# Kernel optimization log

Hardware: AMD Instinct MI355X
Metric: run time of the kernel (lower is better)

## Reference

```python
import jax, jax.numpy as jnp
import numpy as np

BN_EPS = 1e-5
LEAKY_SLOPE = 0.1


def conv_bn_leaky(x, w, gamma, beta, mean, var, pad):
    # Conv2d(no bias) + BatchNorm2d(inference) + LeakyReLU(0.1), NCHW/OIHW
    y = jax.lax.conv_general_dilated(
        x, w, window_strides=(1, 1), padding=[(pad, pad), (pad, pad)],
        dimension_numbers=("NCHW", "OIHW", "NCHW"))
    scale = gamma / jnp.sqrt(var + BN_EPS)
    shift = beta - mean * scale
    y = y * scale[None, :, None, None] + shift[None, :, None, None]
    return jnp.where(y > 0, y, LEAKY_SLOPE * y)


def reorg(x, s=2):
    # vedanet Reorg: out[b, (a*s+d)*C + c, i, j] = x[b, c, i*s+a, j*s+d]
    B, C, H, W = x.shape
    Ho, Wo = H // s, W // s
    return x.reshape(B, C, Ho, s, Wo, s).transpose(0, 3, 5, 1, 2, 4).reshape(B, s * s * C, Ho, Wo)


def setup_inputs() -> dict:
    key = jax.random.key(0)
    ks = jax.random.split(key, 10)
    B, H, W = 32, 19, 19
    NC, NA = 20, 5
    return {
        "stage6": jax.random.normal(ks[0], (B, 1024, H, W), jnp.float32),
        "stage5": jax.random.normal(ks[1], (B, 512, 2 * H, 2 * W), jnp.float32),
        "w1": jax.random.normal(ks[2], (64, 512, 1, 1), jnp.float32) * 0.05,
        "g1": jnp.ones((64,), jnp.float32),
        "b1": jnp.zeros((64,), jnp.float32),
        "m1": jax.random.normal(ks[3], (64,), jnp.float32) * 0.1,
        "v1": jax.random.uniform(ks[4], (64,), jnp.float32, 0.5, 1.5),
        "w2": jax.random.normal(ks[5], (1024, 1280, 3, 3), jnp.float32) * 0.02,
        "g2": jnp.ones((1024,), jnp.float32),
        "b2": jnp.zeros((1024,), jnp.float32),
        "m2": jax.random.normal(ks[6], (1024,), jnp.float32) * 0.1,
        "v2": jax.random.uniform(ks[7], (1024,), jnp.float32, 0.5, 1.5),
        "meta_state": jax.random.normal(ks[8], (NC, NA * 6, 1025), jnp.float32) * 0.05,
    }


def reference(stage6, stage5, w1, g1, b1, m1, v1, w2, g2, b2, m2, v2, meta_state):
    # layers[0]: 1x1 conv-bn-leaky on stage5, then Reorg(2) -> (B, 256, H, W)
    x = conv_bn_leaky(stage5, w1, g1, b1, m1, v1, pad=0)
    x = reorg(x, 2)
    # layers[1]: 3x3 conv-bn-leaky on concat -> (B, 1024, H, W)
    pre = conv_bn_leaky(jnp.concatenate([x, stage6], axis=1), w2, g2, b2, m2, v2, pad=1)
    # meta_predict: per-class 1x1 conv, batched as one einsum
    cls_w = meta_state[:, :, :-1]   # (NC, NA*6, 1024)
    cls_b = meta_state[:, :, -1]    # (NC, NA*6)
    out = jnp.einsum("bkij,cmk->bcmij", pre, cls_w) + cls_b[None, :, :, None, None]
    B, NC, M = pre.shape[0], meta_state.shape[0], meta_state.shape[1]
    return out.reshape(B * NC, M, pre.shape[2], pre.shape[3])
```

## Files before the change

kernel.cpp:

```cpp
#include <hip/hip_runtime.h>

typedef unsigned short u16;
typedef unsigned int   u32;

typedef __attribute__((ext_vector_type(8))) short bf16x8;
typedef __attribute__((ext_vector_type(4))) float f32x4;

__device__ __forceinline__ u16 f2bf(float f) {
  u32 u = __float_as_uint(f);
  u32 r = (u + 0x7fffu + ((u >> 16) & 1u)) >> 16;
  return (u16)r;
}

__device__ __forceinline__ void async16(const void* g, void* l) {
  __builtin_amdgcn_global_load_lds(
      (const __attribute__((address_space(1))) u32*)g,
      (__attribute__((address_space(3))) u32*)l, 16, 0, 0);
}

__global__ __launch_bounds__(256) void mega_prep_kern(
    const float* __restrict__ stage5, const float* __restrict__ s6,
    const float* __restrict__ w1,
    const float* __restrict__ g1, const float* __restrict__ b1,
    const float* __restrict__ m1, const float* __restrict__ v1,
    const float* __restrict__ w2, const float* __restrict__ g2,
    const float* __restrict__ b2, const float* __restrict__ m2,
    const float* __restrict__ v2, const float* __restrict__ meta,
    u16* __restrict__ in_bf, u16* __restrict__ w2p,
    u16* __restrict__ clsp, float* __restrict__ clsb,
    float* __restrict__ shift2)
{
  __shared__ __align__(16) char smem[18816];
  const int bid = blockIdx.x;
  const int t = threadIdx.x;

  if (bid < 722) {
    float* sc_s = (float*)smem;
    float* sh_s = (float*)(smem + 256);
    char*  aT   = smem + 512;
    char*  bT   = smem + 4608;
    const int w = t >> 6, lane = t & 63;
    if (t < 64) {
      float s = g1[t] * rsqrtf(v1[t] + 1e-5f);
      sc_s[t] = s;
      sh_s[t] = b1[t] - m1[t] * s;
    }
    const int m0 = bid * 64;
    const int pS = t & 63, gS = t >> 6;
    const int mS = m0 + pS;
    const int bS = mS / 1444, hwS = mS - bS * 1444;
    const float* s5 = stage5 + (size_t)bS * (512 * 1444) + hwS;
    const int ocA = t >> 2, icqA = t & 3;
    const float* w1r = w1 + (size_t)ocA * 512 + icqA * 8;
    char* aW = aT + (ocA >> 4) * 1024 + (icqA * 16 + (ocA & 15)) * 16;
    char* bW = bT + pS * 64 + ((gS ^ ((pS >> 1) & 3))) * 16;
    const int bR = (w * 16 + (lane & 15)) * 64 +
                   (((lane >> 4) ^ (((lane & 15) >> 1) & 3))) * 16;
    f32x4 acc[4] = {};
    __syncthreads();
    const float sA = sc_s[ocA];
    for (int kc = 0; kc < 16; ++kc) {
      const int ic0 = kc * 32;
      float a8[8], b8[8];
#pragma unroll
      for (int e = 0; e < 8; ++e) a8[e] = w1r[ic0 + e];
#pragma unroll
      for (int e = 0; e < 8; ++e) b8[e] = s5[(size_t)(ic0 + gS * 8 + e) * 1444];
      __syncthreads();
      uint4 av, bv;
      av.x = (u32)f2bf(a8[0] * sA) | ((u32)f2bf(a8[1] * sA) << 16);
      av.y = (u32)f2bf(a8[2] * sA) | ((u32)f2bf(a8[3] * sA) << 16);
      av.z = (u32)f2bf(a8[4] * sA) | ((u32)f2bf(a8[5] * sA) << 16);
      av.w = (u32)f2bf(a8[6] * sA) | ((u32)f2bf(a8[7] * sA) << 16);
      bv.x = (u32)f2bf(b8[0]) | ((u32)f2bf(b8[1]) << 16);
      bv.y = (u32)f2bf(b8[2]) | ((u32)f2bf(b8[3]) << 16);
      bv.z = (u32)f2bf(b8[4]) | ((u32)f2bf(b8[5]) << 16);
      bv.w = (u32)f2bf(b8[6]) | ((u32)f2bf(b8[7]) << 16);
      *(uint4*)aW = av;
      *(uint4*)bW = bv;
      __syncthreads();
      bf16x8 bfv = *(const bf16x8*)(bT + bR);
#pragma unroll
      for (int i = 0; i < 4; ++i) {
        bf16x8 af = *(const bf16x8*)(aT + i * 1024 + lane * 16);
        acc[i] = __builtin_amdgcn_mfma_f32_16x16x32_bf16(af, bfv, acc[i], 0, 0, 0);
      }
    }
    const int mE = m0 + w * 16 + (lane & 15);
    const int bE = mE / 1444, hwE = mE - bE * 1444;
    const int h = hwE / 38, wq = hwE - h * 38;
    const int ho = h >> 1, wo = wq >> 1, q = ((h & 1) << 1) | (wq & 1);
    u16* dst = in_bf + (((size_t)bE * 21 + 1 + ho) * 21 + 1 + wo) * 1280 + q * 64;
    const int lq = lane >> 4;
#pragma unroll
    for (int i = 0; i < 4; ++i) {
      int oc = i * 16 + lq * 4;
      float v0 = acc[i][0] + sh_s[oc + 0]; v0 = v0 > 0.f ? v0 : 0.1f * v0;
      float v1_ = acc[i][1] + sh_s[oc + 1]; v1_ = v1_ > 0.f ? v1_ : 0.1f * v1_;
      float v2_ = acc[i][2] + sh_s[oc + 2]; v2_ = v2_ > 0.f ? v2_ : 0.1f * v2_;
      float v3 = acc[i][3] + sh_s[oc + 3]; v3 = v3 > 0.f ? v3 : 0.1f * v3;
      u32 lo = (u32)f2bf(v0) | ((u32)f2bf(v1_) << 16);
      u32 hi = (u32)f2bf(v2_) | ((u32)f2bf(v3) << 16);
      u32* dp = (u32*)(dst + oc);
      dp[0] = lo; dp[1] = hi;
    }
    return;
  }

  if (bid < 3794) {
    u16 (*tile)[66] = (u16(*)[66])smem;
    const int sub = bid - 722;
    const int jt = sub % 6, ct = (sub / 6) % 16, b = sub / 96;
    const int ij0 = jt * 64, c0 = ct * 64;
    const int col = t & 63, rr = t >> 6;
#pragma unroll
    for (int r = 0; r < 16; ++r) {
      int cl = r * 4 + rr;
      int ij = ij0 + col;
      float v = 0.f;
      if (ij < 361) v = s6[((size_t)b * 1024 + c0 + cl) * 361 + ij];
      tile[cl][col] = f2bf(v);
    }
    __syncthreads();
#pragma unroll
    for (int r = 0; r < 16; ++r) {
      int ijl = r * 4 + rr;
      int ij = ij0 + ijl;
      if (ij < 361) {
        int i = ij / 19, j = ij - i * 19;
        in_bf[(((size_t)b * 21 + 1 + i) * 21 + 1 + j) * 1280 + 256 + c0 + col] =
            tile[col][ijl];
      }
    }
    return;
  }

  if (bid < 5394) {
    int gi = (bid - 3794) * 256 + t;
    int b = gi / 12800;
    int rem = gi - b * 12800;
    int p = rem / 160, qq = rem - p * 160;
    int row, col;
    if (p < 21)      { row = 0;      col = p; }
    else if (p < 42) { row = 20;     col = p - 21; }
    else if (p < 61) { row = p - 41; col = 0; }
    else             { row = p - 60; col = 20; }
    uint4 z = {0u, 0u, 0u, 0u};
    *(uint4*)(in_bf + (((size_t)b * 21 + row) * 21 + col) * 1280 + qq * 8) = z;
    return;
  }

  if (bid < 5694) {
    int idx = (bid - 5394) * 256 + t;
    int cm = idx >> 7, a = idx & 127;
    int kc = a >> 2, ksub = a & 3;
    int tile_ = cm >> 7, g = (cm >> 4) & 7, mm = cm & 15;
    const float* srcp = meta + (size_t)cm * 1025 + a * 8;
    uint4 v;
    v.x = (u32)f2bf(srcp[0]) | ((u32)f2bf(srcp[1]) << 16);
    v.y = (u32)f2bf(srcp[2]) | ((u32)f2bf(srcp[3]) << 16);
    v.z = (u32)f2bf(srcp[4]) | ((u32)f2bf(srcp[5]) << 16);
    v.w = (u32)f2bf(srcp[6]) | ((u32)f2bf(srcp[7]) << 16);
    size_t dst = (((size_t)tile_ * 32 + kc) * 8 + g) * 512
                 + (size_t)(ksub * 16 + mm) * 8;
    *(uint4*)(clsp + dst) = v;
    if (idx < 600) clsb[idx] = meta[(size_t)idx * 1025 + 1024];
    if (idx < 1024) {
      float sc = g2[idx] * rsqrtf(v2[idx] + 1e-5f);
      shift2[idx] = b2[idx] - m2[idx] * sc;
    }
    return;
  }

  {
    u16* tile = (u16*)smem;
    float* sc_s = (float*)(smem + 18720);
    const int sub = bid - 5694;
    const int icb = sub % 10;
    const int oc0 = (sub / 10) * 8;
    if (t < 8) sc_s[t] = g2[oc0 + t] * rsqrtf(v2[oc0 + t] + 1e-5f);
    __syncthreads();
    const float* src = w2 + (size_t)oc0 * 11520 + (size_t)icb * 128 * 9;
#pragma unroll
    for (int r = 0; r < 36; ++r) {
      int p = r * 256 + t;
      int oc_l = p / 1152, rem = p - oc_l * 1152;
      int ic_l = rem / 9, khw = rem - ic_l * 9;
      tile[oc_l * 1170 + khw * 130 + ic_l] =
          f2bf(src[(size_t)oc_l * 11520 + rem] * sc_s[oc_l]);
    }
    __syncthreads();
#pragma unroll
    for (int r = 0; r < 5; ++r) {
      int wi = r * 256 + t;
      if (wi < 1152) {
        int oc_l = wi / 144, q = wi - oc_l * 144;
        int khw = q >> 4, c = (q >> 2) & 3, ksub = q & 3;
        int oc = oc0 + oc_l;
        int kt = khw * 40 + icb * 4 + c;
        const u16* s = &tile[oc_l * 1170 + khw * 130 + c * 32 + ksub * 8];
        uint4 v;
        v.x = (u32)s[0] | ((u32)s[1] << 16);
        v.y = (u32)s[2] | ((u32)s[3] << 16);
        v.z = (u32)s[4] | ((u32)s[5] << 16);
        v.w = (u32)s[6] | ((u32)s[7] << 16);
        size_t dst = (((size_t)(oc >> 8) * 360 + kt) * 2 + ((oc & 255) >> 7)) * 4096
                     + (size_t)(((oc >> 4) & 7) * 64 + ksub * 16 + (oc & 15)) * 8;
        *(uint4*)(w2p + dst) = v;
      }
    }
  }
}

__global__ __launch_bounds__(512, 2) void conv2_gemm_kern(
    const u16* __restrict__ Wp, const u16* __restrict__ Ig,
    const float* __restrict__ shift2, u16* __restrict__ pre)
{
  __shared__ u16 As[4][8192];
  __shared__ u16 Bs[4][8192];
  __shared__ float shft[256];

  const int t = threadIdx.x;
  const int w = t >> 6, lane = t & 63;
  const int wm = w >> 2, wn = w & 3;

  const int s = ((blockIdx.x & 7) * 23) + (blockIdx.x >> 3);
  const int mTile = s >> 2, ocTile = s & 3;
  const int m0 = mTile * 256, oc0 = ocTile * 256;

  const int rw = t >> 2;
  const int rpart = ((t & 3) ^ ((t >> 3) & 3)) * 8;
  int mA = m0 + rw;        if (mA > 11551) mA = 11551;
  int mB = m0 + 128 + rw;  if (mB > 11551) mB = 11551;
  const int bA = mA / 361, ijA = mA - bA * 361;
  const int ohA = ijA / 19, owA = ijA - ohA * 19;
  const int bB = mB / 361, ijB = mB - bB * 361;
  const int ohB = ijB / 19, owB = ijB - ohB * 19;
  const u16* pI0 = Ig + (size_t)((bA * 21 + ohA) * 21 + owA) * 1280 + rpart;
  const u16* pI1 = Ig + (size_t)((bB * 21 + ohB) * 21 + owB) * 1280 + rpart;

  const u16* pW = Wp + (size_t)ocTile * 2949120 + (size_t)t * 8;

  const int aOff = wm * 4096 + lane * 8;
  const int bOff = (wn * 64 + (lane & 15)) * 32 +
                   (((lane >> 4) ^ ((lane >> 1) & 3)) * 8);

  int skh = 0, skw = 0, sicb = 0, sIo = 0;

#pragma unroll
  for (int st = 0; st < 3; ++st) {
    async16(pW + (size_t)st * 8192,        &As[st][t * 8]);
    async16(pI0 + sIo,                     &Bs[st][t * 8]);
    async16(pW + (size_t)st * 8192 + 4096, &As[st][4096 + t * 8]);
    async16(pI1 + sIo,                     &Bs[st][4096 + t * 8]);
    ++sicb; sIo += 32;
    if (sicb == 40) { sicb = 0; ++skw; if (skw == 3) { skw = 0; ++skh; }
                      sIo = (skh * 21 + skw) * 1280; }
  }
  asm volatile("s_waitcnt vmcnt(8)" ::: "memory");
  __builtin_amdgcn_s_barrier();

  f32x4 acc[8][4] = {};

  for (int kt = 0; kt < 360; ++kt) {
    const int cb = kt & 3;
    const u16* Ab = As[cb];
    const u16* Bb = Bs[cb];
    const int stb = (kt + 3) & 3;
    const int st = (kt > 356) ? 359 : kt + 3;
    const size_t aSrc = (size_t)st * 8192;

    bf16x8 af[4], bfv[4];
#pragma unroll
    for (int i = 0; i < 4; ++i)
      af[i] = *(const bf16x8*)&Ab[aOff + i * 512];
#pragma unroll
    for (int j = 0; j < 4; ++j)
      bfv[j] = *(const bf16x8*)&Bb[bOff + j * 512];
    async16(pW + aSrc, &As[stb][t * 8]);
    async16(pI0 + sIo, &Bs[stb][t * 8]);
    __builtin_amdgcn_s_barrier();
    asm volatile("s_waitcnt lgkmcnt(0)" ::: "memory");
    __builtin_amdgcn_sched_barrier(0);
    __builtin_amdgcn_s_setprio(1);
#pragma unroll
    for (int i = 0; i < 4; ++i)
#pragma unroll
      for (int j = 0; j < 4; ++j)
        acc[i][j] = __builtin_amdgcn_mfma_f32_16x16x32_bf16(
            af[i], bfv[j], acc[i][j], 0, 0, 0);
    __builtin_amdgcn_s_setprio(0);
    __builtin_amdgcn_s_barrier();

#pragma unroll
    for (int i = 0; i < 4; ++i)
      af[i] = *(const bf16x8*)&Ab[aOff + 2048 + i * 512];
    async16(pW + aSrc + 4096, &As[stb][4096 + t * 8]);
    async16(pI1 + sIo,        &Bs[stb][4096 + t * 8]);
    __builtin_amdgcn_s_barrier();
    asm volatile("s_waitcnt lgkmcnt(0)" ::: "memory");
    __builtin_amdgcn_sched_barrier(0);
    __builtin_amdgcn_s_setprio(1);
#pragma unroll
    for (int i = 0; i < 4; ++i)
#pragma unroll
      for (int j = 0; j < 4; ++j)
        acc[4 + i][j] = __builtin_amdgcn_mfma_f32_16x16x32_bf16(
            af[i], bfv[j], acc[4 + i][j], 0, 0, 0);
    __builtin_amdgcn_s_setprio(0);
    asm volatile("s_waitcnt vmcnt(8)" ::: "memory");
    __builtin_amdgcn_s_barrier();

    ++sicb; sIo += 32;
    if (sicb == 40) { sicb = 0; ++skw; if (skw == 3) { skw = 0; ++skh; }
                      sIo = (skh * 21 + skw) * 1280; }
  }

  if (t < 256) shft[t] = shift2[oc0 + t];
  __syncthreads();

  const int lq = lane >> 4, lr = lane & 15;
#pragma unroll
  for (int j = 0; j < 4; ++j) {
    const int m = m0 + wn * 64 + j * 16 + lr;
    if (m >= 11552) continue;
    u16* prow = pre + (size_t)m * 1024 + oc0 + wm * 128;
#pragma unroll
    for (int i = 0; i < 8; ++i) {
      const int ocl = i * 16 + lq * 4;
      float v0 = acc[i][j][0] + shft[wm * 128 + ocl + 0]; v0 = v0 > 0.f ? v0 : 0.1f * v0;
      float v1 = acc[i][j][1] + shft[wm * 128 + ocl + 1]; v1 = v1 > 0.f ? v1 : 0.1f * v1;
      float v2 = acc[i][j][2] + shft[wm * 128 + ocl + 2]; v2 = v2 > 0.f ? v2 : 0.1f * v2;
      float v3 = acc[i][j][3] + shft[wm * 128 + ocl + 3]; v3 = v3 > 0.f ? v3 : 0.1f * v3;
      u32 lo = (u32)f2bf(v0) | ((u32)f2bf(v1) << 16);
      u32 hi = (u32)f2bf(v2) | ((u32)f2bf(v3) << 16);
      u32* dp = (u32*)(prow + ocl);
      dp[0] = lo; dp[1] = hi;
    }
  }
}

__global__ __launch_bounds__(256) void einsum_gemm_kern(
    const u16* __restrict__ Ap, const u16* __restrict__ Bg,
    const float* __restrict__ biasg, float* __restrict__ out)
{
  __shared__ u16 Wa[128 * 32];
  __shared__ u16 Ib[128 * 32];
  __shared__ float sbias[128];
  const int t = threadIdx.x;
  const int w = t >> 6, lane = t & 63;
  const int m0 = blockIdx.x * 128;
  const int cm0 = blockIdx.y * 128;
  if (t < 128) { int c = cm0 + t; sbias[t] = (c < 600) ? biasg[c] : 0.f; }

  const u16* pA0 = Ap + ((size_t)(cm0 >> 7) * 256 + w) * 512 + lane * 8;

  const int rw = t >> 2;
  const int rpart = ((t & 3) ^ ((t >> 3) & 3)) * 8;
  int rB0 = m0 + rw;        if (rB0 > 11551) rB0 = 11551;
  int rB1 = m0 + 64 + rw;   if (rB1 > 11551) rB1 = 11551;
  const u16* pB0 = Bg + (size_t)rB0 * 1024 + rpart;
  const u16* pB1 = Bg + (size_t)rB1 * 1024 + rpart;

  u16* waS0 = &Wa[w * 512];
  u16* waS1 = &Wa[2048 + w * 512];
  u16* ibS0 = &Ib[w * 512];
  u16* ibS1 = &Ib[2048 + w * 512];

  const int aBase = (w >> 1) * 2048 + lane * 8;
  const int bBase = (w & 1) * 2048 + (lane & 15) * 32 +
                    (((lane >> 4) ^ ((lane >> 1) & 3))) * 8;

  f32x4 acc[4][4] = {};

  for (int kt = 0; kt < 32; ++kt) {
    const size_t off = (size_t)kt * 32;
    async16(pA0 + (size_t)kt * 4096, waS0);
    async16(pA0 + (size_t)kt * 4096 + 2048, waS1);
    async16(pB0 + off, ibS0);
    async16(pB1 + off, ibS1);
    __syncthreads();
    bf16x8 af[4], bfv[4];
#pragma unroll
    for (int i = 0; i < 4; ++i)
      af[i] = *(const bf16x8*)&Wa[aBase + i * 512];
#pragma unroll
    for (int j = 0; j < 4; ++j)
      bfv[j] = *(const bf16x8*)&Ib[bBase + j * 512];
#pragma unroll
    for (int i = 0; i < 4; ++i)
#pragma unroll
      for (int j = 0; j < 4; ++j)
        acc[i][j] = __builtin_amdgcn_mfma_f32_16x16x32_bf16(
            af[i], bfv[j], acc[i][j], 0, 0, 0);
    __syncthreads();
  }

  const int aRow = (w >> 1) * 64, bRow = (w & 1) * 64;
  const int lq = lane >> 4, lr = lane & 15;
#pragma unroll
  for (int j = 0; j < 4; ++j) {
    int m = m0 + bRow + j * 16 + lr;
    if (m >= 11552) continue;
    int b = m / 361, ij = m - b * 361;
    float* obase = out + (size_t)b * 216600 + ij;
#pragma unroll
    for (int i = 0; i < 4; ++i) {
      int cml = aRow + i * 16 + lq * 4;
#pragma unroll
      for (int r = 0; r < 4; ++r) {
        int cm = cm0 + cml + r;
        if (cm < 600) obase[(size_t)cm * 361] = acc[i][j][r] + sbias[cml + r];
      }
    }
  }
}

extern "C" void kernel_launch(void* const* d_in, const int* in_sizes, int n_in,
                              void* d_out, int out_size, void* d_ws, size_t ws_size,
                              hipStream_t stream)
{
  const float* stage6 = (const float*)d_in[0];
  const float* stage5 = (const float*)d_in[1];
  const float* w1 = (const float*)d_in[2];
  const float* g1 = (const float*)d_in[3];
  const float* b1 = (const float*)d_in[4];
  const float* m1 = (const float*)d_in[5];
  const float* v1 = (const float*)d_in[6];
  const float* w2 = (const float*)d_in[7];
  const float* g2 = (const float*)d_in[8];
  const float* b2 = (const float*)d_in[9];
  const float* m2 = (const float*)d_in[10];
  const float* v2 = (const float*)d_in[11];
  const float* meta = (const float*)d_in[12];
  float* out = (float*)d_out;

  char* ws = (char*)d_ws;
  u16*   in_bf  = (u16*)(ws);
  u16*   w2p    = (u16*)(ws + 36126720);
  u16*   prebf  = (u16*)(ws + 59719680);
  u16*   clsp   = (u16*)(ws + 83378176);
  float* clsb   = (float*)(ws + 84688896);
  float* shift2 = (float*)(ws + 84691456);

  mega_prep_kern<<<6974, 256, 0, stream>>>(
      stage5, stage6, w1, g1, b1, m1, v1, w2, g2, b2, m2, v2, meta,
      in_bf, w2p, clsp, clsb, shift2);
  conv2_gemm_kern<<<184, 512, 0, stream>>>(w2p, in_bf, shift2, prebf);
  einsum_gemm_kern<<<dim3(91, 5), 256, 0, stream>>>(clsp, prebf, clsb, out);
}
```

Before: 584.8 us.

## Shrink conv GEMM M-tile to 192 for more blocks; widen einsum blocks to 512 threads

The conv2 GEMM M-tile drops from 256 to 192 rows, raising the grid from 184 to 244 blocks so more of the 256 CUs are filled. The block-to-XCD mapping is updated for the uneven count, and only half the warps now load the second B half-tile. The einsum GEMM moves to 512-thread blocks covering 256 rows each, which halves the grid and reuses each loaded weight tile across twice as many rows. The trade-off is lower per-block arithmetic intensity in conv2, which means more weight reloads per output, in exchange for better CU utilisation.

```diff
diff --git a/kernel.cpp b/kernel.cpp
--- a/kernel.cpp
+++ b/kernel.cpp
@@ -217,16 +217,17 @@
     const float* __restrict__ shift2, u16* __restrict__ pre)
 {
   __shared__ u16 As[4][8192];
-  __shared__ u16 Bs[4][8192];
+  __shared__ u16 Bs[4][6144];
   __shared__ float shft[256];
 
   const int t = threadIdx.x;
   const int w = t >> 6, lane = t & 63;
   const int wm = w >> 2, wn = w & 3;
 
-  const int s = ((blockIdx.x & 7) * 23) + (blockIdx.x >> 3);
+  const int xcd = blockIdx.x & 7, sub8 = blockIdx.x >> 3;
+  const int s = (xcd < 4 ? xcd * 31 : 124 + (xcd - 4) * 30) + sub8;
   const int mTile = s >> 2, ocTile = s & 3;
-  const int m0 = mTile * 256, oc0 = ocTile * 256;
+  const int m0 = mTile * 192, oc0 = ocTile * 256;
 
   const int rw = t >> 2;
   const int rpart = ((t & 3) ^ ((t >> 3) & 3)) * 8;
@@ -242,7 +243,7 @@
   const u16* pW = Wp + (size_t)ocTile * 2949120 + (size_t)t * 8;
 
   const int aOff = wm * 4096 + lane * 8;
-  const int bOff = (wn * 64 + (lane & 15)) * 32 +
+  const int bOff = (wn * 48 + (lane & 15)) * 32 +
                    (((lane >> 4) ^ ((lane >> 1) & 3)) * 8);
 
   int skh = 0, skw = 0, sicb = 0, sIo = 0;
@@ -252,15 +253,15 @@
     async16(pW + (size_t)st * 8192,        &As[st][t * 8]);
     async16(pI0 + sIo,                     &Bs[st][t * 8]);
     async16(pW + (size_t)st * 8192 + 4096, &As[st][4096 + t * 8]);
-    async16(pI1 + sIo,                     &Bs[st][4096 + t * 8]);
+    if (w < 4) async16(pI1 + sIo,          &Bs[st][4096 + t * 8]);
     ++sicb; sIo += 32;
     if (sicb == 40) { sicb = 0; ++skw; if (skw == 3) { skw = 0; ++skh; }
                       sIo = (skh * 21 + skw) * 1280; }
   }
-  asm volatile("s_waitcnt vmcnt(8)" ::: "memory");
+  asm volatile("s_waitcnt vmcnt(6)" ::: "memory");
   __builtin_amdgcn_s_barrier();
 
-  f32x4 acc[8][4] = {};
+  f32x4 acc[8][3] = {};
 
   for (int kt = 0; kt < 360; ++kt) {
     const int cb = kt & 3;
@@ -270,12 +271,12 @@
     const int st = (kt > 356) ? 359 : kt + 3;
     const size_t aSrc = (size_t)st * 8192;
 
-    bf16x8 af[4], bfv[4];
+    bf16x8 af[4], bfv[3];
 #pragma unroll
     for (int i = 0; i < 4; ++i)
       af[i] = *(const bf16x8*)&Ab[aOff + i * 512];
 #pragma unroll
-    for (int j = 0; j < 4; ++j)
+    for (int j = 0; j < 3; ++j)
       bfv[j] = *(const bf16x8*)&Bb[bOff + j * 512];
     async16(pW + aSrc, &As[stb][t * 8]);
     async16(pI0 + sIo, &Bs[stb][t * 8]);
@@ -286,7 +287,7 @@
 #pragma unroll
     for (int i = 0; i < 4; ++i)
 #pragma unroll
-      for (int j = 0; j < 4; ++j)
+      for (int j = 0; j < 3; ++j)
         acc[i][j] = __builtin_amdgcn_mfma_f32_16x16x32_bf16(
             af[i], bfv[j], acc[i][j], 0, 0, 0);
     __builtin_amdgcn_s_setprio(0);
@@ -296,7 +297,7 @@
     for (int i = 0; i < 4; ++i)
       af[i] = *(const bf16x8*)&Ab[aOff + 2048 + i * 512];
     async16(pW + aSrc + 4096, &As[stb][4096 + t * 8]);
-    async16(pI1 + sIo,        &Bs[stb][4096 + t * 8]);
+    if (w < 4) async16(pI1 + sIo, &Bs[stb][4096 + t * 8]);
     __builtin_amdgcn_s_barrier();
     asm volatile("s_waitcnt lgkmcnt(0)" ::: "memory");
     __builtin_amdgcn_sched_barrier(0);
@@ -304,11 +305,11 @@
 #pragma unroll
     for (int i = 0; i < 4; ++i)
 #pragma unroll
-      for (int j = 0; j < 4; ++j)
+      for (int j = 0; j < 3; ++j)
         acc[4 + i][j] = __builtin_amdgcn_mfma_f32_16x16x32_bf16(
             af[i], bfv[j], acc[4 + i][j], 0, 0, 0);
     __builtin_amdgcn_s_setprio(0);
-    asm volatile("s_waitcnt vmcnt(8)" ::: "memory");
+    asm volatile("s_waitcnt vmcnt(6)" ::: "memory");
     __builtin_amdgcn_s_barrier();
 
     ++sicb; sIo += 32;
@@ -321,8 +322,8 @@
 
   const int lq = lane >> 4, lr = lane & 15;
 #pragma unroll
-  for (int j = 0; j < 4; ++j) {
-    const int m = m0 + wn * 64 + j * 16 + lr;
+  for (int j = 0; j < 3; ++j) {
+    const int m = m0 + wn * 48 + j * 16 + lr;
     if (m >= 11552) continue;
     u16* prow = pre + (size_t)m * 1024 + oc0 + wm * 128;
 #pragma unroll
@@ -340,45 +341,40 @@
   }
 }
 
-__global__ __launch_bounds__(256) void einsum_gemm_kern(
+__global__ __launch_bounds__(512) void einsum_gemm_kern(
     const u16* __restrict__ Ap, const u16* __restrict__ Bg,
     const float* __restrict__ biasg, float* __restrict__ out)
 {
-  __shared__ u16 Wa[128 * 32];
-  __shared__ u16 Ib[128 * 32];
+  __shared__ u16 Wa[4096];
+  __shared__ u16 Ib[8192];
   __shared__ float sbias[128];
   const int t = threadIdx.x;
   const int w = t >> 6, lane = t & 63;
-  const int m0 = blockIdx.x * 128;
+  const int q = w >> 1, ch = w & 1;
+  const int m0 = blockIdx.x * 256;
   const int cm0 = blockIdx.y * 128;
   if (t < 128) { int c = cm0 + t; sbias[t] = (c < 600) ? biasg[c] : 0.f; }
 
-  const u16* pA0 = Ap + ((size_t)(cm0 >> 7) * 256 + w) * 512 + lane * 8;
+  const u16* pA = Ap + (size_t)(cm0 >> 7) * (32 * 4096) + (size_t)t * 8;
 
   const int rw = t >> 2;
   const int rpart = ((t & 3) ^ ((t >> 3) & 3)) * 8;
   int rB0 = m0 + rw;        if (rB0 > 11551) rB0 = 11551;
-  int rB1 = m0 + 64 + rw;   if (rB1 > 11551) rB1 = 11551;
+  int rB1 = m0 + 128 + rw;  if (rB1 > 11551) rB1 = 11551;
   const u16* pB0 = Bg + (size_t)rB0 * 1024 + rpart;
   const u16* pB1 = Bg + (size_t)rB1 * 1024 + rpart;
 
-  u16* waS0 = &Wa[w * 512];
-  u16* waS1 = &Wa[2048 + w * 512];
-  u16* ibS0 = &Ib[w * 512];
-  u16* ibS1 = &Ib[2048 + w * 512];
-
-  const int aBase = (w >> 1) * 2048 + lane * 8;
-  const int bBase = (w & 1) * 2048 + (lane & 15) * 32 +
+  const int aBase = ch * 2048 + lane * 8;
+  const int bBase = (q * 64 + (lane & 15)) * 32 +
                     (((lane >> 4) ^ ((lane >> 1) & 3))) * 8;
 
   f32x4 acc[4][4] = {};
 
   for (int kt = 0; kt < 32; ++kt) {
     const size_t off = (size_t)kt * 32;
-    async16(pA0 + (size_t)kt * 4096, waS0);
-    async16(pA0 + (size_t)kt * 4096 + 2048, waS1);
-    async16(pB0 + off, ibS0);
-    async16(pB1 + off, ibS1);
+    async16(pA + (size_t)kt * 4096, &Wa[t * 8]);
+    async16(pB0 + off, &Ib[t * 8]);
+    async16(pB1 + off, &Ib[4096 + t * 8]);
     __syncthreads();
     bf16x8 af[4], bfv[4];
 #pragma unroll
@@ -396,17 +392,16 @@
     __syncthreads();
   }
 
-  const int aRow = (w >> 1) * 64, bRow = (w & 1) * 64;
   const int lq = lane >> 4, lr = lane & 15;
 #pragma unroll
   for (int j = 0; j < 4; ++j) {
-    int m = m0 + bRow + j * 16 + lr;
+    int m = m0 + q * 64 + j * 16 + lr;
     if (m >= 11552) continue;
     int b = m / 361, ij = m - b * 361;
     float* obase = out + (size_t)b * 216600 + ij;
 #pragma unroll
     for (int i = 0; i < 4; ++i) {
-      int cml = aRow + i * 16 + lq * 4;
+      int cml = ch * 64 + i * 16 + lq * 4;
 #pragma unroll
       for (int r = 0; r < 4; ++r) {
         int cm = cm0 + cml + r;
@@ -446,6 +441,6 @@
   mega_prep_kern<<<6974, 256, 0, stream>>>(
       stage5, stage6, w1, g1, b1, m1, v1, w2, g2, b2, m2, v2, meta,
       in_bf, w2p, clsp, clsb, shift2);
-  conv2_gemm_kern<<<184, 512, 0, stream>>>(w2p, in_bf, shift2, prebf);
-  einsum_gemm_kern<<<dim3(91, 5), 256, 0, stream>>>(clsp, prebf, clsb, out);
-}
+  conv2_gemm_kern<<<244, 512, 0, stream>>>(w2p, in_bf, shift2, prebf);
+  einsum_gemm_kern<<<dim3(46, 5), 512, 0, stream>>>(clsp, prebf, clsb, out);
+}
```

Result: faster. 550.7 us (-5.8%).
